# Performance work log

Measured on AMD Instinct MI355X. Metric: run time of the kernel, lower is better.

Reference implementation:

```python
import jax, jax.numpy as jnp
import numpy as np

B, D, S, SE, H, DFF = 4, 1024, 1024, 1024, 16, 4096
DH = D // H
NUDGE = 1e-7


def norm(x):
    # x: [B, D, S]; custom layer norm: mean over (1,2), then divide by full L2 norm
    size = x.shape[1] * x.shape[2]
    mean = jnp.sum(x, axis=(1, 2)) / size
    x = x - mean[:, None, None]
    std = jnp.sqrt(jnp.sum(x * x, axis=(1, 2)))
    return x / (std[:, None, None] + NUDGE)


def mha(q_in, kv_in, Wq, Wk, Wv, Wo, causal):
    # q_in: [B, Sq, D], kv_in: [B, Sk, D]
    Bq, Sq, _ = q_in.shape
    Sk = kv_in.shape[1]
    q = (q_in @ Wq).reshape(Bq, Sq, H, DH)
    k = (kv_in @ Wk).reshape(Bq, Sk, H, DH)
    v = (kv_in @ Wv).reshape(Bq, Sk, H, DH)
    scores = jnp.einsum('bqhd,bkhd->bhqk', q, k) / jnp.sqrt(jnp.asarray(DH, q.dtype))
    if causal:
        mask = jnp.tril(jnp.ones((Sq, Sk), dtype=bool))
        scores = jnp.where(mask, scores, jnp.finfo(scores.dtype).min)
    attn = jax.nn.softmax(scores, axis=-1)
    out = jnp.einsum('bhqk,bkhd->bqhd', attn, v).reshape(Bq, Sq, D)
    return out @ Wo


def setup_inputs() -> dict:
    key = jax.random.key(0)
    ks = jax.random.split(key, 13)
    w = lambda k, sh: jax.random.normal(k, sh, dtype=jnp.float32) * 0.02
    return {
        'embedding': jax.random.normal(ks[0], (B, D, SE), dtype=jnp.float32),
        'other_inputs': jax.random.normal(ks[1], (B, D, S), dtype=jnp.float32),
        'Wq_s': w(ks[2], (D, D)), 'Wk_s': w(ks[3], (D, D)),
        'Wv_s': w(ks[4], (D, D)), 'Wo_s': w(ks[5], (D, D)),
        'Wq_c': w(ks[6], (D, D)), 'Wk_c': w(ks[7], (D, D)),
        'Wv_c': w(ks[8], (D, D)), 'Wo_c': w(ks[9], (D, D)),
        'W1': w(ks[10], (D, DFF)), 'b1': jnp.zeros((DFF,), jnp.float32),
        'W2': w(ks[11], (DFF, D)), 'b2': jnp.zeros((D,), jnp.float32),
    }


def reference(embedding, other_inputs, Wq_s, Wk_s, Wv_s, Wo_s,
              Wq_c, Wk_c, Wv_c, Wo_c, W1, b1, W2, b2):
    # tensors are [B, D, S]; attention operates on [B, S, D]
    x = other_inputs.transpose(0, 2, 1)
    sa = mha(x, x, Wq_s, Wk_s, Wv_s, Wo_s, causal=True)
    post_attention = norm(other_inputs + sa.transpose(0, 2, 1))

    pa = post_attention.transpose(0, 2, 1)
    emb = embedding.transpose(0, 2, 1)
    ca = mha(pa, emb, Wq_c, Wk_c, Wv_c, Wo_c, causal=False)
    post_embedding = norm(post_attention + ca.transpose(0, 2, 1))

    # per-token MLP (original loops over axis 2 and restacks; here fully batched)
    pe = post_embedding.transpose(0, 2, 1)  # [B, S, D]
    ff = jax.nn.relu(pe @ W1 + b1) @ W2 + b2
    return norm(post_embedding + ff.transpose(0, 2, 1))
```

## Files before the change

### kernel.cpp

```cpp
#include <hip/hip_runtime.h>
#include <cmath>

#define B_   4
#define D_   1024
#define S_   1024
#define H_   16
#define DH_  64
#define DFF_ 4096

typedef __attribute__((ext_vector_type(8))) short bf16x8;
typedef __attribute__((ext_vector_type(4))) float f32x4;

__device__ __forceinline__ unsigned short f2b(float f) {
    unsigned int u = __float_as_uint(f);
    u += 0x7fffu + ((u >> 16) & 1u);
    return (unsigned short)(u >> 16);
}

__device__ __forceinline__ void gload_lds16(const unsigned short* g, unsigned short* l) {
    __builtin_amdgcn_global_load_lds(
        (const __attribute__((address_space(1))) void*)g,
        (__attribute__((address_space(3))) void*)l, 16, 0, 0);
}

template <int BN>
__global__ __launch_bounds__(512, 2)
void gemm8(const unsigned short* __restrict__ A,
           const unsigned short* __restrict__ Wt,
           const float* __restrict__ bias,
           float* __restrict__ Cf, unsigned short* __restrict__ Cb,
           int N, int K, int lda, int ldb, long csplit, int relu)
{
    constexpr int BM = 256;
    constexpr int FM = 8, FN = BN / 64;
    constexpr int ACALLS = BM / 64, BCALLS = BN / 64;
    constexpr int L = ACALLS + BCALLS;
    constexpr int ASZ = BM * 64, BSZ = BN * 64;
    __shared__ unsigned short lds[2 * (ASZ + BSZ)];

    const int tid = threadIdx.x;
    const int w = tid >> 6, lane = tid & 63;
    const int quad = lane >> 4, l16 = lane & 15;
    const int m0 = blockIdx.x * BM, n0 = blockIdx.y * BN;
    const int wm = (w >> 2) * 128;
    const int wn = (w & 3) * (BN / 4);
    const int srow = lane >> 3;
    const int scol = ((lane & 7) ^ srow) * 8;

    A  += (size_t)blockIdx.z * K;
    Wt += (size_t)blockIdx.z * K;
    if (Cf) Cf += (size_t)blockIdx.z * csplit;

    const int nt = K >> 6;

    auto STAGE = [&](int t, int buf) {
        const int k0 = t << 6;
        unsigned short* As = lds + buf * (ASZ + BSZ);
        unsigned short* Bs = As + ASZ;
#pragma unroll
        for (int i = 0; i < ACALLS; ++i) {
            const int inst = w + 8 * i;
            gload_lds16(A + (size_t)(m0 + inst * 8 + srow) * lda + k0 + scol,
                        As + inst * 512);
        }
#pragma unroll
        for (int i = 0; i < BCALLS; ++i) {
            const int inst = w + 8 * i;
            gload_lds16(Wt + (size_t)(n0 + inst * 8 + srow) * ldb + k0 + scol,
                        Bs + inst * 512);
        }
    };

    f32x4 acc[FM][FN] = {};

    STAGE(0, 0);
    STAGE(1, 1);
    asm volatile("s_waitcnt vmcnt(%0)\n\ts_barrier" :: "i"(L) : "memory");

    int cur = 0;
    for (int t = 0; t < nt; ++t) {
        const unsigned short* As = lds + cur * (ASZ + BSZ);
        const unsigned short* Bs = As + ASZ;
#pragma unroll
        for (int kk = 0; kk < 2; ++kk) {
            bf16x8 af[FM], bfr[FN];
#pragma unroll
            for (int i = 0; i < FM; ++i) {
                const int r = wm + i * 16 + l16;
                af[i] = *(const bf16x8*)&As[r * 64 + (((kk * 4 + quad) ^ (r & 7)) * 8)];
            }
#pragma unroll
            for (int j = 0; j < FN; ++j) {
                const int r = wn + j * 16 + l16;
                bfr[j] = *(const bf16x8*)&Bs[r * 64 + (((kk * 4 + quad) ^ (r & 7)) * 8)];
            }
            __builtin_amdgcn_s_setprio(1);
#pragma unroll
            for (int i = 0; i < FM; ++i)
#pragma unroll
                for (int j = 0; j < FN; ++j)
                    acc[i][j] = __builtin_amdgcn_mfma_f32_16x16x32_bf16(af[i], bfr[j], acc[i][j], 0, 0, 0);
            __builtin_amdgcn_s_setprio(0);
        }
        if (t == nt - 1) break;
        asm volatile("s_barrier" ::: "memory");
        if (t + 2 < nt) {
            STAGE(t + 2, cur);
            asm volatile("s_waitcnt vmcnt(%0)\n\ts_barrier" :: "i"(L) : "memory");
        } else {
            asm volatile("s_waitcnt vmcnt(0)\n\ts_barrier" ::: "memory");
        }
        cur ^= 1;
    }

#pragma unroll
    for (int i = 0; i < FM; ++i) {
        const int grow = m0 + wm + i * 16 + quad * 4;
#pragma unroll
        for (int j = 0; j < FN; ++j) {
            const int gcol = n0 + wn + j * 16 + l16;
            const float bv = bias ? bias[gcol] : 0.f;
#pragma unroll
            for (int r = 0; r < 4; ++r) {
                float vv = acc[i][j][r] + bv;
                if (relu) vv = fmaxf(vv, 0.f);
                if (Cf) Cf[(size_t)(grow + r) * N + gcol] = vv;
                if (Cb) Cb[(size_t)(grow + r) * N + gcol] = f2b(vv);
            }
        }
    }
}

template <int BM, int BN, bool RES>
__global__ __launch_bounds__(256, 2)
void gemm_t(const unsigned short* __restrict__ A,
            const unsigned short* __restrict__ Wt,
            const float* __restrict__ bias,
            const float* __restrict__ residual,
            float* __restrict__ Cf, unsigned short* __restrict__ Cb,
            float* __restrict__ partial,
            int N, int K, int lda, int ldb, long csplit, int relu)
{
    constexpr int FM = BM / 32, FN = BN / 32;
    __shared__ unsigned short As[BM * 64];
    __shared__ unsigned short Bs[BN * 64];
    const int tid = threadIdx.x;
    const int w = tid >> 6, lane = tid & 63;
    const int quad = lane >> 4, l16 = lane & 15;
    const int m0 = blockIdx.x * BM, n0 = blockIdx.y * BN;
    const int wm = (w >> 1) * (BM / 2), wn = (w & 1) * (BN / 2);
    const int srow = lane >> 3;
    const int scol = ((lane & 7) ^ srow) * 8;

    A  += (size_t)blockIdx.z * K;
    Wt += (size_t)blockIdx.z * K;
    if (Cf) Cf += (size_t)blockIdx.z * csplit;

    f32x4 acc[FM][FN] = {};

    for (int k0 = 0; k0 < K; k0 += 64) {
#pragma unroll
        for (int i = 0; i < BM / 32; ++i) {
            const int inst = w + 4 * i;
            gload_lds16(A + (size_t)(m0 + inst * 8 + srow) * lda + k0 + scol,
                        As + inst * 512);
        }
#pragma unroll
        for (int i = 0; i < BN / 32; ++i) {
            const int inst = w + 4 * i;
            gload_lds16(Wt + (size_t)(n0 + inst * 8 + srow) * ldb + k0 + scol,
                        Bs + inst * 512);
        }
        __syncthreads();

#pragma unroll
        for (int kk = 0; kk < 2; ++kk) {
            bf16x8 af[FM], bfr[FN];
#pragma unroll
            for (int i = 0; i < FM; ++i) {
                const int r = wm + i * 16 + l16;
                af[i] = *(const bf16x8*)&As[r * 64 + (((kk * 4 + quad) ^ (r & 7)) * 8)];
            }
#pragma unroll
            for (int j = 0; j < FN; ++j) {
                const int r = wn + j * 16 + l16;
                bfr[j] = *(const bf16x8*)&Bs[r * 64 + (((kk * 4 + quad) ^ (r & 7)) * 8)];
            }
#pragma unroll
            for (int i = 0; i < FM; ++i)
#pragma unroll
                for (int j = 0; j < FN; ++j)
                    acc[i][j] = __builtin_amdgcn_mfma_f32_16x16x32_bf16(af[i], bfr[j], acc[i][j], 0, 0, 0);
        }
        __syncthreads();
    }

    float s = 0.f, ss = 0.f;
#pragma unroll
    for (int i = 0; i < FM; ++i) {
        const int grow = m0 + wm + i * 16 + quad * 4;
#pragma unroll
        for (int j = 0; j < FN; ++j) {
            const int gcol = n0 + wn + j * 16 + l16;
            const float bv = bias ? bias[gcol] : 0.f;
#pragma unroll
            for (int r = 0; r < 4; ++r) {
                float vv = acc[i][j][r] + bv;
                if (relu) vv = fmaxf(vv, 0.f);
                if constexpr (RES) {
                    vv += residual[(size_t)(grow + r) * N + gcol];
                    s += vv; ss += vv * vv;
                    Cf[(size_t)(grow + r) * N + gcol] = vv;
                } else {
                    if (Cf) Cf[(size_t)(grow + r) * N + gcol] = vv;
                    if (Cb) Cb[(size_t)(grow + r) * N + gcol] = f2b(vv);
                }
            }
        }
    }

    if constexpr (RES) {
        float* rs = (float*)As;
        float* rss = rs + 256;
        rs[tid] = s; rss[tid] = ss;
        __syncthreads();
        for (int off = 128; off > 0; off >>= 1) {
            if (tid < off) { rs[tid] += rs[tid + off]; rss[tid] += rss[tid + off]; }
            __syncthreads();
        }
        if (tid == 0) {
            constexpr int YPB = S_ / BM;
            const int b = blockIdx.x / YPB;
            const int chunk = (blockIdx.x % YPB) * gridDim.y + blockIdx.y;
            const int chunks = YPB * gridDim.y;
            partial[((size_t)b * chunks + chunk) * 2 + 0] = rs[0];
            partial[((size_t)b * chunks + chunk) * 2 + 1] = rss[0];
        }
    }
}

__global__ void reduce2_res(const float* __restrict__ pc, const float* __restrict__ res,
                            const float* __restrict__ bias, float* __restrict__ y,
                            float* __restrict__ partial)
{
    const size_t pcs = (size_t)4096 * 1024;
    const int b = blockIdx.y;
    const size_t base = (size_t)b * 1048576 + (size_t)blockIdx.x * 16384;
    float s = 0.f, ss = 0.f;
    for (int i = threadIdx.x; i < 4096; i += 256) {
        const size_t e = base + (size_t)i * 4;
        float4 v0 = *(const float4*)&pc[e];
        float4 v1 = *(const float4*)&pc[e + pcs];
        float4 rv = *(const float4*)&res[e];
        float4 bv = *(const float4*)&bias[e & 1023];
        float4 o;
        o.x = v0.x + v1.x + rv.x + bv.x;
        o.y = v0.y + v1.y + rv.y + bv.y;
        o.z = v0.z + v1.z + rv.z + bv.z;
        o.w = v0.w + v1.w + rv.w + bv.w;
        *(float4*)&y[e] = o;
        s += o.x + o.y + o.z + o.w;
        ss += o.x * o.x + o.y * o.y + o.z * o.z + o.w * o.w;
    }
    __shared__ float rs[256], rss[256];
    rs[threadIdx.x] = s; rss[threadIdx.x] = ss;
    __syncthreads();
    for (int off = 128; off > 0; off >>= 1) {
        if (threadIdx.x < off) {
            rs[threadIdx.x] += rs[threadIdx.x + off];
            rss[threadIdx.x] += rss[threadIdx.x + off];
        }
        __syncthreads();
    }
    if (threadIdx.x == 0) {
        partial[((size_t)b * 64 + blockIdx.x) * 2 + 0] = rs[0];
        partial[((size_t)b * 64 + blockIdx.x) * 2 + 1] = rss[0];
    }
}

__device__ __forceinline__ void stats_reduce(const float* __restrict__ partial,
                                             int b, int chunks, int tid,
                                             float* rs, float* rss,
                                             float& mean, float& inv)
{
    float s = 0.f, ss = 0.f;
    for (int i = tid; i < chunks; i += 256) {
        s  += partial[((size_t)b * chunks + i) * 2 + 0];
        ss += partial[((size_t)b * chunks + i) * 2 + 1];
    }
    rs[tid] = s; rss[tid] = ss;
    __syncthreads();
    for (int off = 128; off > 0; off >>= 1) {
        if (tid < off) { rs[tid] += rs[tid + off]; rss[tid] += rss[tid + off]; }
        __syncthreads();
    }
    const float size = (float)(D_ * S_);
    const float m = rs[0] / size;
    const float var = fmaxf(rss[0] - size * m * m, 0.f);
    mean = m;
    inv = 1.f / (sqrtf(var) + 1e-7f);
    __syncthreads();
}

__global__ void norm_apply_dual(float* __restrict__ y, unsigned short* __restrict__ yb,
                                const float* __restrict__ partial, int chunks)
{
    __shared__ float rs[256], rss[256];
    const int b = blockIdx.y;
    float mean, inv;
    stats_reduce(partial, b, chunks, threadIdx.x, rs, rss, mean, inv);

    const int perBatch = D_ * S_;
    float4* y4 = (float4*)(y + (size_t)b * perBatch);
    unsigned short* yb_ = yb + (size_t)b * perBatch;
    const int n4 = perBatch / 4;
    for (int i = blockIdx.x * blockDim.x + threadIdx.x; i < n4;
         i += gridDim.x * blockDim.x) {
        float4 v = y4[i];
        v.x = (v.x - mean) * inv; v.y = (v.y - mean) * inv;
        v.z = (v.z - mean) * inv; v.w = (v.w - mean) * inv;
        y4[i] = v;
        ushort4 hh; hh.x = f2b(v.x); hh.y = f2b(v.y); hh.z = f2b(v.z); hh.w = f2b(v.w);
        *(ushort4*)(yb_ + (size_t)i * 4) = hh;
    }
}

template <bool CAUSAL>
__global__ __launch_bounds__(512, 4)
void attn_mfma3(const unsigned short* __restrict__ q, const unsigned short* __restrict__ k,
                const unsigned short* __restrict__ vt, unsigned short* __restrict__ o,
                int qstride, int kstride)
{
    __shared__ unsigned short Ks[128 * 64];
    __shared__ unsigned short Vt[64 * 128];
    __shared__ unsigned short Ps[8][16][72];
    const int tid = threadIdx.x;
    const int w = tid >> 6, lane = tid & 63;
    const int quad = lane >> 4, l16 = lane & 15;
    const int h = blockIdx.y, b = blockIdx.z;
    const int qt = CAUSAL ? ((blockIdx.x + h) & 7) : blockIdx.x;
    const int q0 = qt * 128;
    const int row0 = q0 + w * 16;

    const int ksr = lane >> 3, ksc = ((lane & 7) ^ (lane >> 3)) * 8;
    const int vsr = lane >> 4, vsc = lane & 15;

    const unsigned short* qA = q + (size_t)(b * S_ + row0 + l16) * qstride + h * DH_;
    const bf16x8 qa0 = *(const bf16x8*)(qA + quad * 8);
    const bf16x8 qa1 = *(const bf16x8*)(qA + 32 + quad * 8);

    f32x4 OA[4] = {};
    float lA[4] = {};

    const int nit = CAUSAL ? (qt + 1) : (S_ / 128);
    for (int t = 0; t < nit; ++t) {
        const int j0 = t * 128;
#pragma unroll
        for (int i = 0; i < 2; ++i) {
            const int ins = w + 8 * i;
            gload_lds16(k + (size_t)(b * S_ + j0 + ins * 8 + ksr) * kstride + h * DH_ + ksc,
                        Ks + ins * 512);
            const int vrow = ins * 4 + vsr;
            gload_lds16(vt + (size_t)((b * H_ + h) * DH_ + vrow) * S_ + j0
                           + ((vsc ^ (vrow & 15)) * 8),
                        Vt + ins * 512);
        }
        __syncthreads();

#pragma unroll
        for (int g = 0; g < 2; ++g) {
            const int jg = j0 + g * 64;
            const bool doW = !CAUSAL || (jg <= row0 + 15);
            const bool needMask = CAUSAL && doW && (jg + 63 > row0);

            if (doW) {
                f32x4 stA[4];
#pragma unroll
                for (int n = 0; n < 4; ++n) {
                    const int kr = g * 64 + n * 16 + l16;
                    const bf16x8 kf0 = *(const bf16x8*)&Ks[kr * 64 + ((quad ^ (kr & 7)) * 8)];
                    const bf16x8 kf1 = *(const bf16x8*)&Ks[kr * 64 + (((quad + 4) ^ (kr & 7)) * 8)];
                    f32x4 c = {};
                    c = __builtin_amdgcn_mfma_f32_16x16x32_bf16(qa0, kf0, c, 0, 0, 0);
                    c = __builtin_amdgcn_mfma_f32_16x16x32_bf16(qa1, kf1, c, 0, 0, 0);
                    stA[n] = c;
                }

#pragma unroll
                for (int n = 0; n < 4; ++n)
#pragma unroll
                    for (int r = 0; r < 4; ++r) {
                        float sv = stA[n][r] * 0.125f;
                        if (needMask) {
                            const int row = row0 + quad * 4 + r;
                            const int key = jg + n * 16 + l16;
                            if (key > row) sv = -1e30f;
                        }
                        const float p = __expf(sv);
                        lA[r] += p;
                        Ps[w][quad * 4 + r][n * 16 + l16] = f2b(p);
                    }
                __threadfence_block();

                const bf16x8 pa0 = *(const bf16x8*)&Ps[w][l16][quad * 8];
                const bf16x8 pa1 = *(const bf16x8*)&Ps[w][l16][32 + quad * 8];
#pragma unroll
                for (int n = 0; n < 4; ++n) {
                    const int vr = n * 16 + l16;
                    const bf16x8 vf0 = *(const bf16x8*)&Vt[vr * 128 + (((g * 8 + quad) ^ l16) * 8)];
                    const bf16x8 vf1 = *(const bf16x8*)&Vt[vr * 128 + (((g * 8 + quad + 4) ^ l16) * 8)];
                    OA[n] = __builtin_amdgcn_mfma_f32_16x16x32_bf16(pa0, vf0, OA[n], 0, 0, 0);
                    OA[n] = __builtin_amdgcn_mfma_f32_16x16x32_bf16(pa1, vf1, OA[n], 0, 0, 0);
                }
            }
        }
        __syncthreads();
    }

#pragma unroll
    for (int r = 0; r < 4; ++r) {
        float la = lA[r];
        la += __shfl_xor(la, 1); la += __shfl_xor(la, 2);
        la += __shfl_xor(la, 4); la += __shfl_xor(la, 8);
        const float ia = 1.f / la;
        const size_t baseA = (size_t)(b * S_ + row0 + quad * 4 + r) * D_ + h * DH_;
#pragma unroll
        for (int n = 0; n < 4; ++n)
            o[baseA + n * 16 + l16] = f2b(OA[n][r] * ia);
    }
}

__global__ void transpose_v(const unsigned short* __restrict__ src,
                            unsigned short* __restrict__ dst, int istride)
{
    __shared__ unsigned short t[32][34];
    const int z = blockIdx.z, b = z >> 4, h = z & 15;
    const int s0 = blockIdx.x * 32, d0 = blockIdx.y * 32;
    const int tx = threadIdx.x, ty = threadIdx.y;
#pragma unroll
    for (int i = 0; i < 4; ++i)
        t[ty + i * 8][tx] =
            src[(size_t)(b * S_ + s0 + ty + i * 8) * istride + h * DH_ + d0 + tx];
    __syncthreads();
#pragma unroll
    for (int i = 0; i < 4; ++i)
        dst[(size_t)(z * DH_ + d0 + ty + i * 8) * S_ + s0 + tx] = t[tx][ty + i * 8];
}

struct WJob { const float* src; int sld; long doff; int dld; };
struct WJobs { WJob j[16]; };

__global__ void wtrans_all(WJobs js, unsigned short* __restrict__ dst)
{
    __shared__ float tile[32][33];
    const WJob J = js.j[blockIdx.z];
    const int c0 = blockIdx.x * 32, r0 = blockIdx.y * 32;
    const int tx = threadIdx.x, ty = threadIdx.y;
#pragma unroll
    for (int i = 0; i < 4; ++i)
        tile[ty + i * 8][tx] = J.src[(size_t)(r0 + ty + i * 8) * J.sld + c0 + tx];
    __syncthreads();
#pragma unroll
    for (int i = 0; i < 4; ++i)
        dst[J.doff + (size_t)(c0 + ty + i * 8) * J.dld + r0 + tx] =
            f2b(tile[tx][ty + i * 8]);
}

__global__ void transpose_in(const float* __restrict__ other, const float* __restrict__ emb,
                             float* __restrict__ f0, unsigned short* __restrict__ xb,
                             unsigned short* __restrict__ eb)
{
    __shared__ float tile[32][33];
    const int z = blockIdx.z;
    const int b = z & 3;
    const bool isEmb = z >= 4;
    const float* ip = (isEmb ? emb : other) + (size_t)b * 1048576;
    const int c0 = blockIdx.x * 32, r0 = blockIdx.y * 32;
    const int tx = threadIdx.x, ty = threadIdx.y;
#pragma unroll
    for (int i = 0; i < 4; ++i)
        tile[ty + i * 8][tx] = ip[(size_t)(r0 + ty + i * 8) * 1024 + c0 + tx];
    __syncthreads();
#pragma unroll
    for (int i = 0; i < 4; ++i) {
        const float v = tile[tx][ty + i * 8];
        const size_t oidx = (size_t)b * 1048576 + (size_t)(c0 + ty + i * 8) * 1024 + r0 + tx;
        if (isEmb) eb[oidx] = f2b(v);
        else { f0[oidx] = v; xb[oidx] = f2b(v); }
    }
}

__global__ void transpose_out(const float* __restrict__ in, float* __restrict__ outf,
                              const float* __restrict__ partial, int chunks)
{
    __shared__ float tile[32][33];
    __shared__ float rs[256], rss[256];
    const int z = blockIdx.z;
    const int tx = threadIdx.x, ty = threadIdx.y;
    const int tid = ty * 32 + tx;

    float mean, inv;
    stats_reduce(partial, z, chunks, tid, rs, rss, mean, inv);

    const float* ip = in + (size_t)z * 1048576;
    const int c0 = blockIdx.x * 32, r0 = blockIdx.y * 32;
#pragma unroll
    for (int i = 0; i < 4; ++i)
        tile[ty + i * 8][tx] = ip[(size_t)(r0 + ty + i * 8) * 1024 + c0 + tx];
    __syncthreads();
#pragma unroll
    for (int i = 0; i < 4; ++i) {
        const float v = (tile[tx][ty + i * 8] - mean) * inv;
        outf[(size_t)z * 1048576 + (size_t)(c0 + ty + i * 8) * 1024 + r0 + tx] = v;
    }
}

extern "C" void kernel_launch(void* const* d_in, const int* in_sizes, int n_in,
                              void* d_out, int out_size, void* d_ws, size_t ws_size,
                              hipStream_t stream)
{
    const float* embedding = (const float*)d_in[0];
    const float* other     = (const float*)d_in[1];
    const float* W1 = (const float*)d_in[10];
    const float* b1 = (const float*)d_in[11];
    const float* W2 = (const float*)d_in[12];
    const float* b2 = (const float*)d_in[13];
    float* out = (float*)d_out;

    char* wsb = (char*)d_ws;
    const size_t MB = 1u << 20;
    float* f0 = (float*)(wsb + 0 * MB);
    float* f2 = (float*)(wsb + 16 * MB);
    unsigned short* wts  = (unsigned short*)(wsb + 32 * MB);
    unsigned short* wqkv = wts;
    unsigned short* wo_s = wts + 3 * 1048576;
    unsigned short* wq_c = wts + 4 * 1048576;
    unsigned short* wkv_c= wts + 5 * 1048576;
    unsigned short* wo_c = wts + 7 * 1048576;
    unsigned short* w1t  = wts + 8 * 1048576;
    unsigned short* w2t  = wts + 12 * 1048576;
    unsigned short* actA = (unsigned short*)(wsb + 64 * MB);
    unsigned short* actB = (unsigned short*)(wsb + 72 * MB);
    unsigned short* actC = (unsigned short*)(wsb + 80 * MB);
    unsigned short* actC2 = actC + 4 * 1048576;
    unsigned short* aout  = actC + 12 * 1048576;
    float* pc      = (float*)(wsb + 112 * MB);
    float* partial = (float*)(wsb + 176 * MB);

    const dim3 blkT(32, 8), blk256(256), blk512(512);
    const dim3 gAttn(S_ / 128, H_, B_);
    const dim3 gVt(32, 2, B_ * H_);
    const dim3 gApply(64, B_);

    WJobs js;
    for (int z = 0; z < 8; ++z)
        js.j[z] = { (const float*)d_in[2 + z], 1024, (long)z * 1048576, 1024 };
    for (int q = 0; q < 4; ++q)
        js.j[8 + q] = { W1 + (size_t)q * 1024, 4096, (long)(8 + q) * 1048576, 1024 };
    for (int q = 0; q < 4; ++q)
        js.j[12 + q] = { W2 + (size_t)q * 1048576, 1024, 12L * 1048576 + q * 1024, 4096 };
    hipLaunchKernelGGL(wtrans_all, dim3(32, 32, 16), blkT, 0, stream, js, wts);

    hipLaunchKernelGGL(transpose_in, dim3(32, 32, 8), blkT, 0, stream,
                       other, embedding, f0, actA, actB);

    hipLaunchKernelGGL((gemm8<256>), dim3(16, 12), blk512, 0, stream,
                       actA, wqkv, nullptr, nullptr, actC,
                       3072, 1024, 1024, 1024, 0L, 0);
    hipLaunchKernelGGL(transpose_v, gVt, blkT, 0, stream, actC + 2048, actA, 3072);
    hipLaunchKernelGGL(attn_mfma3<true>, gAttn, blk512, 0, stream,
                       actC, actC + 1024, actA, aout, 3072, 3072);
    hipLaunchKernelGGL((gemm_t<64, 128, true>), dim3(64, 8), blk256, 0, stream,
                       aout, wo_s, nullptr, f0, f2, nullptr, partial,
                       1024, 1024, 1024, 1024, 0L, 0);
    hipLaunchKernelGGL(norm_apply_dual, gApply, blk256, 0, stream, f2, actA, partial, 128);

    hipLaunchKernelGGL((gemm_t<64, 128, false>), dim3(64, 8), blk256, 0, stream,
                       actA, wq_c, nullptr, nullptr, nullptr, actC, nullptr,
                       1024, 1024, 1024, 1024, 0L, 0);
    hipLaunchKernelGGL((gemm8<128>), dim3(16, 16), blk512, 0, stream,
                       actB, wkv_c, nullptr, nullptr, actC2,
                       2048, 1024, 1024, 1024, 0L, 0);
    hipLaunchKernelGGL(transpose_v, gVt, blkT, 0, stream, actC2 + 1024, actB, 2048);
    hipLaunchKernelGGL(attn_mfma3<false>, gAttn, blk512, 0, stream,
                       actC, actC2, actB, aout, 1024, 2048);
    hipLaunchKernelGGL((gemm_t<64, 128, true>), dim3(64, 8), blk256, 0, stream,
                       aout, wo_c, nullptr, f2, f0, nullptr, partial,
                       1024, 1024, 1024, 1024, 0L, 0);
    hipLaunchKernelGGL(norm_apply_dual, gApply, blk256, 0, stream, f0, actA, partial, 128);

    hipLaunchKernelGGL((gemm8<256>), dim3(16, 16), blk512, 0, stream,
                       actA, w1t, b1, nullptr, actC,
                       DFF_, 1024, 1024, 1024, 0L, 1);
    hipLaunchKernelGGL((gemm8<128>), dim3(16, 8, 2), blk512, 0, stream,
                       actC, w2t, nullptr, pc, nullptr,
                       1024, 2048, 4096, 4096, (long)4096 * 1024, 0);
    hipLaunchKernelGGL(reduce2_res, gApply, blk256, 0, stream, pc, f0, b2, f2, partial);
    hipLaunchKernelGGL(transpose_out, dim3(32, 32, B_), blkT, 0, stream, f2, out, partial, 64);

    (void)in_sizes; (void)n_in; (void)out_size; (void)ws_size;
}
```

Baseline: 478.3 us.

## Add phased, prefetch-interleaved 256x256 GEMM and use split-K of four for the FFN down-projection

Adds a new bf16 MFMA GEMM, gemm8p, with 256x256 tiles and double-buffered LDS. The A tile for step t+1 and the B tile for step t+2 are issued in quarter chunks, interleaved between four MFMA phases, with barriers and raised wave priority around each compute phase. The aim is to hide global-to-LDS latency behind the matrix math. The self-attention QKV, W1 and W2 GEMMs now use this kernel. The W2 GEMM moves from a two-way to a four-way K split, and the residual reduction now sums four partials. This raises the partial-buffer traffic and footprint, and the extra barriers and a larger register footprint could limit occupancy.

```diff
diff --git a/kernel.cpp b/kernel.cpp
--- a/kernel.cpp
+++ b/kernel.cpp
@@ -21,6 +21,125 @@
     __builtin_amdgcn_global_load_lds(
         (const __attribute__((address_space(1))) void*)g,
         (__attribute__((address_space(3))) void*)l, 16, 0, 0);
+}
+
+#define GP_PHASE(Q, ...)                                                       \
+    {                                                                          \
+        bf16x8 af[2][2];                                                       \
+        _Pragma("unroll") for (int i = 0; i < 2; ++i)                          \
+            _Pragma("unroll") for (int kk = 0; kk < 2; ++kk) {                 \
+                const int r = wm + (2 * (Q) + i) * 16 + l16;                   \
+                af[i][kk] = *(const bf16x8*)&As[r * 64 + (((kk * 4 + quad) ^ (r & 7)) * 8)]; \
+            }                                                                  \
+        __VA_ARGS__;                                                           \
+        asm volatile("s_barrier" ::: "memory");                                \
+        asm volatile("s_waitcnt lgkmcnt(0)" ::: "memory");                     \
+        __builtin_amdgcn_sched_barrier(0);                                     \
+        __builtin_amdgcn_s_setprio(1);                                         \
+        _Pragma("unroll") for (int kk = 0; kk < 2; ++kk)                       \
+            _Pragma("unroll") for (int i = 0; i < 2; ++i)                      \
+                _Pragma("unroll") for (int j = 0; j < 4; ++j)                  \
+                    acc[2 * (Q) + i][j] = __builtin_amdgcn_mfma_f32_16x16x32_bf16( \
+                        af[i][kk], bfr[j][kk], acc[2 * (Q) + i][j], 0, 0, 0);  \
+        __builtin_amdgcn_s_setprio(0);                                         \
+    }
+
+__global__ __launch_bounds__(512, 2)
+void gemm8p(const unsigned short* __restrict__ A,
+            const unsigned short* __restrict__ Wt,
+            const float* __restrict__ bias,
+            float* __restrict__ Cf, unsigned short* __restrict__ Cb,
+            int N, int K, int lda, int ldb, long csplit, int relu)
+{
+    constexpr int BM = 256, BN = 256;
+    constexpr int SLOT = (BM + BN) * 64;
+    __shared__ unsigned short lds[2 * SLOT];
+
+    const int tid = threadIdx.x;
+    const int w = tid >> 6, lane = tid & 63;
+    const int quad = lane >> 4, l16 = lane & 15;
+    const int m0 = blockIdx.x * BM, n0 = blockIdx.y * BN;
+    const int wm = (w >> 2) * 128, wn = (w & 3) * 64;
+    const int srow = lane >> 3;
+    const int scol = ((lane & 7) ^ srow) * 8;
+
+    A  += (size_t)blockIdx.z * K;
+    Wt += (size_t)blockIdx.z * K;
+    if (Cf) Cf += (size_t)blockIdx.z * csplit;
+
+    const int nt = K >> 6;
+
+    auto stageA = [&](int t, int ht) {
+        unsigned short* dst = lds + (t & 1) * SLOT;
+        const int k0 = t << 6;
+#pragma unroll
+        for (int i = 0; i < 2; ++i) {
+            const int g = ht * 16 + w * 2 + i;
+            gload_lds16(A + (size_t)(m0 + g * 8 + srow) * lda + k0 + scol,
+                        dst + g * 512);
+        }
+    };
+    auto stageB = [&](int t, int ht) {
+        unsigned short* dst = lds + (t & 1) * SLOT + BM * 64;
+        const int k0 = t << 6;
+#pragma unroll
+        for (int i = 0; i < 2; ++i) {
+            const int g = ht * 16 + w * 2 + i;
+            gload_lds16(Wt + (size_t)(n0 + g * 8 + srow) * ldb + k0 + scol,
+                        dst + g * 512);
+        }
+    };
+
+    f32x4 acc[8][4] = {};
+    bf16x8 bfr[4][2];
+
+    stageA(0, 0); stageA(0, 1); stageB(0, 0); stageB(0, 1);
+    stageB(1, 0); stageB(1, 1);
+    asm volatile("s_waitcnt vmcnt(4)\n\ts_barrier" ::: "memory");
+
+    for (int t = 0; ; ) {
+        const unsigned short* As = lds + (t & 1) * SLOT;
+        const unsigned short* Bs = As + BM * 64;
+        const bool sA = (t + 1 < nt), sB = (t + 2 < nt);
+
+#pragma unroll
+        for (int j = 0; j < 4; ++j)
+#pragma unroll
+            for (int kk = 0; kk < 2; ++kk) {
+                const int r = wn + j * 16 + l16;
+                bfr[j][kk] = *(const bf16x8*)&Bs[r * 64 + (((kk * 4 + quad) ^ (r & 7)) * 8)];
+            }
+        GP_PHASE(0, if (sA) stageA(t + 1, 0));
+        asm volatile("s_barrier" ::: "memory");
+        GP_PHASE(1, if (sA) stageA(t + 1, 1));
+        asm volatile("s_barrier" ::: "memory");
+        GP_PHASE(2, if (sB) stageB(t + 2, 0));
+        asm volatile("s_barrier" ::: "memory");
+        GP_PHASE(3, if (sB) stageB(t + 2, 1));
+
+        if (++t == nt) break;
+        if (t + 1 < nt)
+            asm volatile("s_waitcnt vmcnt(4)\n\ts_barrier" ::: "memory");
+        else
+            asm volatile("s_waitcnt vmcnt(0)\n\ts_barrier" ::: "memory");
+    }
+
+#pragma unroll
+    for (int i = 0; i < 8; ++i) {
+        const int grow = m0 + wm + i * 16 + quad * 4;
+#pragma unroll
+        for (int j = 0; j < 4; ++j) {
+            const int gcol = n0 + wn + j * 16 + l16;
+            const float bv = bias ? bias[gcol] : 0.f;
+#pragma unroll
+            for (int r = 0; r < 4; ++r) {
+                float vv = acc[i][j][r] + bv;
+                if (relu) vv = fmaxf(vv, 0.f);
+                if (Cf) Cf[(size_t)(grow + r) * N + gcol] = vv;
+                if (Cb) Cb[(size_t)(grow + r) * N + gcol] = f2b(vv);
+            }
+        }
+    }
 }
 
 template <int BN>
@@ -251,13 +370,15 @@
         const size_t e = base + (size_t)i * 4;
         float4 v0 = *(const float4*)&pc[e];
         float4 v1 = *(const float4*)&pc[e + pcs];
+        float4 v2 = *(const float4*)&pc[e + 2 * pcs];
+        float4 v3 = *(const float4*)&pc[e + 3 * pcs];
         float4 rv = *(const float4*)&res[e];
         float4 bv = *(const float4*)&bias[e & 1023];
         float4 o;
-        o.x = v0.x + v1.x + rv.x + bv.x;
-        o.y = v0.y + v1.y + rv.y + bv.y;
-        o.z = v0.z + v1.z + rv.z + bv.z;
-        o.w = v0.w + v1.w + rv.w + bv.w;
+        o.x = v0.x + v1.x + v2.x + v3.x + rv.x + bv.x;
+        o.y = v0.y + v1.y + v2.y + v3.y + rv.y + bv.y;
+        o.z = v0.z + v1.z + v2.z + v3.z + rv.z + bv.z;
+        o.w = v0.w + v1.w + v2.w + v3.w + rv.w + bv.w;
         *(float4*)&y[e] = o;
         s += o.x + o.y + o.z + o.w;
         ss += o.x * o.x + o.y * o.y + o.z * o.z + o.w * o.w;
@@ -564,7 +685,7 @@
     hipLaunchKernelGGL(transpose_in, dim3(32, 32, 8), blkT, 0, stream,
                        other, embedding, f0, actA, actB);
 
-    hipLaunchKernelGGL((gemm8<256>), dim3(16, 12), blk512, 0, stream,
+    hipLaunchKernelGGL(gemm8p, dim3(16, 12), blk512, 0, stream,
                        actA, wqkv, nullptr, nullptr, actC,
                        3072, 1024, 1024, 1024, 0L, 0);
     hipLaunchKernelGGL(transpose_v, gVt, blkT, 0, stream, actC + 2048, actA, 3072);
@@ -589,12 +710,12 @@
                        1024, 1024, 1024, 1024, 0L, 0);
     hipLaunchKernelGGL(norm_apply_dual, gApply, blk256, 0, stream, f0, actA, partial, 128);
 
-    hipLaunchKernelGGL((gemm8<256>), dim3(16, 16), blk512, 0, stream,
+    hipLaunchKernelGGL(gemm8p, dim3(16, 16), blk512, 0, stream,
                        actA, w1t, b1, nullptr, actC,
                        DFF_, 1024, 1024, 1024, 0L, 1);
-    hipLaunchKernelGGL((gemm8<128>), dim3(16, 8, 2), blk512, 0, stream,
+    hipLaunchKernelGGL(gemm8p, dim3(16, 4, 4), blk512, 0, stream,
                        actC, w2t, nullptr, pc, nullptr,
-                       1024, 2048, 4096, 4096, (long)4096 * 1024, 0);
+                       1024, 1024, 4096, 4096, (long)4096 * 1024, 0);
     hipLaunchKernelGGL(reduce2_res, gApply, blk256, 0, stream, pc, f0, b2, f2, partial);
     hipLaunchKernelGGL(transpose_out, dim3(32, 32, B_), blkT, 0, stream, f2, out, partial, 64);
 
```

New measurement: 482.7 us. About the same (+0.9%).
